# Kernel tuning notes

Measured on AMD Instinct MI355X. Metric: run time of the kernel, lower is better.

Reference implementation:

```python
import jax, jax.numpy as jnp
import numpy as np

NUM_GRAPHS = 512  # static number of segments (graphs in the batch)
EPS = 1e-05


def setup_inputs() -> dict:
    key = jax.random.key(0)
    k1, k2 = jax.random.split(key)
    N, C = 500000, 128
    x = jax.random.normal(k1, (N, C), dtype=jnp.float32)
    batch = jnp.sort(jax.random.randint(k2, (N,), 0, NUM_GRAPHS)).astype(jnp.int64)
    weight = jnp.ones((C,), dtype=jnp.float32)
    bias = jnp.zeros((C,), dtype=jnp.float32)
    return {"x": x, "batch": batch, "weight": weight, "bias": bias}


def reference(x, batch, weight, bias):
    # Per-graph mean/var over nodes (dim=0 within each graph), per channel.
    seg = batch.astype(jnp.int32)
    counts = jax.ops.segment_sum(jnp.ones((x.shape[0],), x.dtype), seg,
                                 num_segments=NUM_GRAPHS)  # [B]
    counts = jnp.maximum(counts, 1.0)[:, None]             # guard empty graphs
    sums = jax.ops.segment_sum(x, seg, num_segments=NUM_GRAPHS)          # [B, C]
    sqsums = jax.ops.segment_sum(x * x, seg, num_segments=NUM_GRAPHS)    # [B, C]
    mean = sums / counts                                   # [B, C]
    var = sqsums / counts - mean * mean                    # biased (unbiased=False)
    inv_std = jax.lax.rsqrt(var + EPS)
    out = (x - mean[seg]) * inv_std[seg]                   # gather per node
    return out * weight + bias
```

## Files before the change

kernel.cpp:

```cpp
#include <hip/hip_runtime.h>

#define NUM_GRAPHS 512
#define EPS 1e-5f
#define CHN 128
#define CHN4 32
#define PORTIONS 8

__device__ __forceinline__ int lower_bound_i(const int* __restrict__ b, int n, int val) {
    int l = 0, r = n;
    while (l < r) {
        int m = (l + r) >> 1;
        if (b[m] < val) l = m + 1; else r = m;
    }
    return l;
}

__global__ __launch_bounds__(256) void gln_stage1(
    const float* __restrict__ x,
    const int* __restrict__ batch,
    float* __restrict__ ws_part,
    int N)
{
    const int s   = blockIdx.x >> 3;
    const int p   = blockIdx.x & (PORTIONS - 1);
    const int tid = threadIdx.x;
    const int q   = tid & 31;
    const int g   = tid >> 5;

    const int lo = lower_bound_i(batch, N, s);
    const int hi = lower_bound_i(batch, N, s + 1);

    const float4* __restrict__ x4 = (const float4*)x;

    float4 sum = make_float4(0.f, 0.f, 0.f, 0.f);
    float4 sq  = make_float4(0.f, 0.f, 0.f, 0.f);
    for (int row = lo + p * 8 + g; row < hi; row += 64) {
        float4 v = x4[(size_t)row * CHN4 + q];
        sum.x += v.x; sum.y += v.y; sum.z += v.z; sum.w += v.w;
        sq.x  += v.x * v.x; sq.y += v.y * v.y; sq.z += v.z * v.z; sq.w += v.w * v.w;
    }

    __shared__ float4 s_sum[256];
    __shared__ float4 s_sq[256];
    s_sum[tid] = sum; s_sq[tid] = sq;
    __syncthreads();

    for (int off = 128; off >= 32; off >>= 1) {
        if (tid < off) {
            float4 a = s_sum[tid], b = s_sum[tid + off];
            a.x += b.x; a.y += b.y; a.z += b.z; a.w += b.w;
            s_sum[tid] = a;
            float4 c = s_sq[tid], d = s_sq[tid + off];
            c.x += d.x; c.y += d.y; c.z += d.z; c.w += d.w;
            s_sq[tid] = c;
        }
        __syncthreads();
    }

    float4* out4 = (float4*)ws_part + (size_t)blockIdx.x * 64;
    if (tid < 32) out4[tid] = s_sum[tid];
    else if (tid < 64) out4[tid] = s_sq[tid - 32];
}

__global__ __launch_bounds__(128) void gln_finalize(
    const float* __restrict__ ws_part,
    const int* __restrict__ batch,
    const float* __restrict__ weight,
    const float* __restrict__ bias,
    float* __restrict__ ws_stats,
    int N)
{
    const int s = blockIdx.x;
    const int c = threadIdx.x;

    const int lo = lower_bound_i(batch, N, s);
    const int hi = lower_bound_i(batch, N, s + 1);

    float sum = 0.f, sq = 0.f;
    const float* base = ws_part + (size_t)s * PORTIONS * 256;
    #pragma unroll
    for (int p = 0; p < PORTIONS; ++p) {
        sum += base[p * 256 + c];
        sq  += base[p * 256 + 128 + c];
    }
    float inv_cnt = 1.f / fmaxf((float)(hi - lo), 1.f);
    float mean = sum * inv_cnt;
    float inv_std = rsqrtf(sq * inv_cnt - mean * mean + EPS);
    float scale = inv_std * weight[c];
    float shift = bias[c] - mean * scale;
    ws_stats[(size_t)s * 256 + c]       = scale;
    ws_stats[(size_t)s * 256 + 128 + c] = shift;
}

__global__ __launch_bounds__(256) void gln_normalize(
    const float* __restrict__ x,
    const int* __restrict__ batch,
    const float* __restrict__ ws_stats,
    float* __restrict__ out,
    int N)
{
    const float4* __restrict__ x4 = (const float4*)x;
    const float4* __restrict__ st4 = (const float4*)ws_stats;
    float4* __restrict__ o4 = (float4*)out;

    const size_t total = (size_t)N * CHN4;
    size_t e = (size_t)blockIdx.x * blockDim.x + threadIdx.x;
    const size_t stride = (size_t)gridDim.x * blockDim.x;

    for (; e < total; e += stride) {
        int row = (int)(e >> 5);
        int q   = (int)(e & 31);
        int seg = batch[row];
        float4 sc = st4[(size_t)seg * 64 + q];
        float4 sh = st4[(size_t)seg * 64 + 32 + q];
        float4 v  = x4[e];
        float4 r;
        r.x = fmaf(v.x, sc.x, sh.x);
        r.y = fmaf(v.y, sc.y, sh.y);
        r.z = fmaf(v.z, sc.z, sh.z);
        r.w = fmaf(v.w, sc.w, sh.w);
        o4[e] = r;
    }
}

extern "C" void kernel_launch(void* const* d_in, const int* in_sizes, int n_in,
                              void* d_out, int out_size, void* d_ws, size_t ws_size,
                              hipStream_t stream) {
    const float* x      = (const float*)d_in[0];
    const int*   batch  = (const int*)d_in[1];
    const float* weight = (const float*)d_in[2];
    const float* bias   = (const float*)d_in[3];
    float*       out    = (float*)d_out;
    const int N = in_sizes[0] / CHN;

    float* ws_part  = (float*)d_ws;
    float* ws_stats = ws_part + (size_t)NUM_GRAPHS * PORTIONS * 256;

    gln_stage1<<<NUM_GRAPHS * PORTIONS, 256, 0, stream>>>(x, batch, ws_part, N);
    gln_finalize<<<NUM_GRAPHS, 128, 0, stream>>>(ws_part, batch, weight, bias, ws_stats, N);

    const size_t total4 = (size_t)N * CHN4;
    int nblocks = (int)((total4 + 256 * 4 - 1) / (256 * 4));
    gln_normalize<<<nblocks, 256, 0, stream>>>(x, batch, ws_stats, out, N);
}
```

Before: 490.9 us.

## Precompute segment offsets, fuse stats with finalize, and row-tile normalize with cached scale

A small kernel now computes the segment offsets once by binary search, replacing the repeated searches in every block. The partial-sum and finalize kernels are merged into one 1024-thread block per graph that reduces and writes scale/shift directly, which removes a launch and a workspace round trip. Normalize processes contiguous row tiles and caches scale/shift per segment instead of reloading batch and stats for every element. It also uses nontemporal loads and stores. Having only 512 blocks for the stats pass may reduce the memory parallelism available for the first full read of x.

```diff
diff --git a/kernel.cpp b/kernel.cpp
--- a/kernel.cpp
+++ b/kernel.cpp
@@ -4,7 +4,9 @@
 #define EPS 1e-5f
 #define CHN 128
 #define CHN4 32
-#define PORTIONS 8
+#define RPB 256
+
+typedef float f32x4 __attribute__((ext_vector_type(4)));
 
 __device__ __forceinline__ int lower_bound_i(const int* __restrict__ b, int n, int val) {
     int l = 0, r = n;
@@ -15,37 +17,46 @@
     return l;
 }
 
-__global__ __launch_bounds__(256) void gln_stage1(
+__global__ __launch_bounds__(128) void gln_offsets(
+    const int* __restrict__ batch, int* __restrict__ seg_off, int N)
+{
+    int s = blockIdx.x * 128 + threadIdx.x;
+    if (s < NUM_GRAPHS)       seg_off[s] = lower_bound_i(batch, N, s);
+    else if (s == NUM_GRAPHS) seg_off[s] = N;
+}
+
+__global__ __launch_bounds__(1024) void gln_stats(
     const float* __restrict__ x,
-    const int* __restrict__ batch,
-    float* __restrict__ ws_part,
-    int N)
+    const int* __restrict__ seg_off,
+    const float* __restrict__ weight,
+    const float* __restrict__ bias,
+    float* __restrict__ ws_stats)
 {
-    const int s   = blockIdx.x >> 3;
-    const int p   = blockIdx.x & (PORTIONS - 1);
+    const int s   = blockIdx.x;
     const int tid = threadIdx.x;
     const int q   = tid & 31;
     const int g   = tid >> 5;
 
-    const int lo = lower_bound_i(batch, N, s);
-    const int hi = lower_bound_i(batch, N, s + 1);
+    const int lo = seg_off[s];
+    const int hi = seg_off[s + 1];
 
     const float4* __restrict__ x4 = (const float4*)x;
 
     float4 sum = make_float4(0.f, 0.f, 0.f, 0.f);
     float4 sq  = make_float4(0.f, 0.f, 0.f, 0.f);
-    for (int row = lo + p * 8 + g; row < hi; row += 64) {
-        float4 v = x4[(size_t)row * CHN4 + q];
+    for (int r = lo + g; r < hi; r += 32) {
+        float4 v = x4[(size_t)r * CHN4 + q];
         sum.x += v.x; sum.y += v.y; sum.z += v.z; sum.w += v.w;
         sq.x  += v.x * v.x; sq.y += v.y * v.y; sq.z += v.z * v.z; sq.w += v.w * v.w;
     }
 
-    __shared__ float4 s_sum[256];
-    __shared__ float4 s_sq[256];
+    __shared__ float4 s_sum[1024];
+    __shared__ float4 s_sq[1024];
     s_sum[tid] = sum; s_sq[tid] = sq;
     __syncthreads();
 
-    for (int off = 128; off >= 32; off >>= 1) {
+    #pragma unroll
+    for (int off = 512; off >= 32; off >>= 1) {
         if (tid < off) {
             float4 a = s_sum[tid], b = s_sum[tid + off];
             a.x += b.x; a.y += b.y; a.z += b.z; a.w += b.w;
@@ -57,69 +68,58 @@
         __syncthreads();
     }
 
-    float4* out4 = (float4*)ws_part + (size_t)blockIdx.x * 64;
-    if (tid < 32) out4[tid] = s_sum[tid];
-    else if (tid < 64) out4[tid] = s_sq[tid - 32];
-}
-
-__global__ __launch_bounds__(128) void gln_finalize(
-    const float* __restrict__ ws_part,
-    const int* __restrict__ batch,
-    const float* __restrict__ weight,
-    const float* __restrict__ bias,
-    float* __restrict__ ws_stats,
-    int N)
-{
-    const int s = blockIdx.x;
-    const int c = threadIdx.x;
-
-    const int lo = lower_bound_i(batch, N, s);
-    const int hi = lower_bound_i(batch, N, s + 1);
-
-    float sum = 0.f, sq = 0.f;
-    const float* base = ws_part + (size_t)s * PORTIONS * 256;
-    #pragma unroll
-    for (int p = 0; p < PORTIONS; ++p) {
-        sum += base[p * 256 + c];
-        sq  += base[p * 256 + 128 + c];
+    if (tid < CHN) {
+        float sum_c = ((const float*)s_sum)[tid];
+        float sq_c  = ((const float*)s_sq)[tid];
+        float inv_cnt = 1.f / fmaxf((float)(hi - lo), 1.f);
+        float mean    = sum_c * inv_cnt;
+        float inv_std = rsqrtf(sq_c * inv_cnt - mean * mean + EPS);
+        float scale = inv_std * weight[tid];
+        float shift = bias[tid] - mean * scale;
+        ws_stats[(size_t)s * 256 + tid]       = scale;
+        ws_stats[(size_t)s * 256 + 128 + tid] = shift;
     }
-    float inv_cnt = 1.f / fmaxf((float)(hi - lo), 1.f);
-    float mean = sum * inv_cnt;
-    float inv_std = rsqrtf(sq * inv_cnt - mean * mean + EPS);
-    float scale = inv_std * weight[c];
-    float shift = bias[c] - mean * scale;
-    ws_stats[(size_t)s * 256 + c]       = scale;
-    ws_stats[(size_t)s * 256 + 128 + c] = shift;
 }
 
 __global__ __launch_bounds__(256) void gln_normalize(
     const float* __restrict__ x,
     const int* __restrict__ batch,
+    const int* __restrict__ seg_off,
     const float* __restrict__ ws_stats,
-    float* __restrict__ out,
-    int N)
+    float* __restrict__ out, int N)
 {
-    const float4* __restrict__ x4 = (const float4*)x;
+    const int tid = threadIdx.x;
+    const int q   = tid & 31;
+    const int g   = tid >> 5;
+
+    const int row0 = blockIdx.x * RPB + g;
+    const int rend = min(blockIdx.x * RPB + RPB, N);
+    if (row0 >= rend) return;
+
+    int seg = batch[row0];
+    int hi  = seg_off[seg + 1];
+
     const float4* __restrict__ st4 = (const float4*)ws_stats;
-    float4* __restrict__ o4 = (float4*)out;
+    float4 sc = st4[(size_t)seg * 64 + q];
+    float4 sh = st4[(size_t)seg * 64 + 32 + q];
 
-    const size_t total = (size_t)N * CHN4;
-    size_t e = (size_t)blockIdx.x * blockDim.x + threadIdx.x;
-    const size_t stride = (size_t)gridDim.x * blockDim.x;
+    const f32x4* __restrict__ x4 = (const f32x4*)x;
+    f32x4* __restrict__ o4       = (f32x4*)out;
 
-    for (; e < total; e += stride) {
-        int row = (int)(e >> 5);
-        int q   = (int)(e & 31);
-        int seg = batch[row];
-        float4 sc = st4[(size_t)seg * 64 + q];
-        float4 sh = st4[(size_t)seg * 64 + 32 + q];
-        float4 v  = x4[e];
-        float4 r;
-        r.x = fmaf(v.x, sc.x, sh.x);
-        r.y = fmaf(v.y, sc.y, sh.y);
-        r.z = fmaf(v.z, sc.z, sh.z);
-        r.w = fmaf(v.w, sc.w, sh.w);
-        o4[e] = r;
+    for (int r = row0; r < rend; r += 8) {
+        while (r >= hi) {
+            ++seg;
+            hi = seg_off[seg + 1];
+            sc = st4[(size_t)seg * 64 + q];
+            sh = st4[(size_t)seg * 64 + 32 + q];
+        }
+        const f32x4 v = __builtin_nontemporal_load(x4 + ((size_t)r * CHN4 + q));
+        f32x4 o;
+        o.x = fmaf(v.x, sc.x, sh.x);
+        o.y = fmaf(v.y, sc.y, sh.y);
+        o.z = fmaf(v.z, sc.z, sh.z);
+        o.w = fmaf(v.w, sc.w, sh.w);
+        __builtin_nontemporal_store(o, o4 + ((size_t)r * CHN4 + q));
     }
 }
 
@@ -133,13 +133,10 @@
     float*       out    = (float*)d_out;
     const int N = in_sizes[0] / CHN;
 
-    float* ws_part  = (float*)d_ws;
-    float* ws_stats = ws_part + (size_t)NUM_GRAPHS * PORTIONS * 256;
+    int*   seg_off  = (int*)d_ws;
+    float* ws_stats = (float*)((char*)d_ws + 4096);
 
-    gln_stage1<<<NUM_GRAPHS * PORTIONS, 256, 0, stream>>>(x, batch, ws_part, N);
-    gln_finalize<<<NUM_GRAPHS, 128, 0, stream>>>(ws_part, batch, weight, bias, ws_stats, N);
-
-    const size_t total4 = (size_t)N * CHN4;
-    int nblocks = (int)((total4 + 256 * 4 - 1) / (256 * 4));
-    gln_normalize<<<nblocks, 256, 0, stream>>>(x, batch, ws_stats, out, N);
+    gln_offsets<<<(NUM_GRAPHS + 1 + 127) / 128, 128, 0, stream>>>(batch, seg_off, N);
+    gln_stats<<<NUM_GRAPHS, 1024, 0, stream>>>(x, seg_off, weight, bias, ws_stats);
+    gln_normalize<<<(N + RPB - 1) / RPB, 256, 0, stream>>>(x, batch, seg_off, ws_stats, out, N);
 }
```

New measurement: 474.2 us. 1.04x faster.
